# Kernel optimization log

Measured on AMD Instinct MI355X. Metric: run time of the kernel, lower is better.

The kernel has to match this reference:

```python
import jax, jax.numpy as jnp
import numpy as np

N = 50000          # nodes
E = 800000         # edges (before self-loops)
DIN = 1024         # input_dim_mel
HID = 128          # hidden_dim
HEADS = 2
NC = 4             # num_classes
NEG_SLOPE = 0.2    # PyG GATConv default


def setup_inputs() -> dict:
    key = jax.random.key(0)
    ks = jax.random.split(key, 12)
    s = 0.05
    return {
        "x": jax.random.normal(ks[0], (N, DIN), dtype=jnp.float32),
        "edge_index": jax.random.randint(ks[1], (2, E), 0, N, dtype=jnp.int64),
        # linear_pre (stored as [in, out])
        "W_pre": jax.random.normal(ks[2], (DIN, HID), dtype=jnp.float32) * s,
        "b_pre": jnp.zeros((HID,), dtype=jnp.float32),
        # gat1: GATConv(HID, HID, heads=2, concat=True)
        "W1": jax.random.normal(ks[3], (HID, HEADS * HID), dtype=jnp.float32) * s,
        "a_src1": jax.random.normal(ks[4], (HEADS, HID), dtype=jnp.float32) * s,
        "a_dst1": jax.random.normal(ks[5], (HEADS, HID), dtype=jnp.float32) * s,
        "b1": jnp.zeros((HEADS * HID,), dtype=jnp.float32),
        # gat2: GATConv(HID*HEADS, NC, heads=1, concat=True)
        "W2": jax.random.normal(ks[6], (HEADS * HID, NC), dtype=jnp.float32) * s,
        "a_src2": jax.random.normal(ks[7], (1, NC), dtype=jnp.float32) * s,
        "a_dst2": jax.random.normal(ks[8], (1, NC), dtype=jnp.float32) * s,
        "b2": jnp.zeros((NC,), dtype=jnp.float32),
    }


def _gat_conv(x, W, a_src, a_dst, bias, src, dst, heads, out_ch):
    """PyG GATConv (concat=True, self-loops already appended to src/dst)."""
    n = x.shape[0]
    h = (x @ W).reshape(n, heads, out_ch)            # [N,H,C]
    alpha_src = (h * a_src).sum(-1)                  # [N,H]
    alpha_dst = (h * a_dst).sum(-1)                  # [N,H]
    e = alpha_src[src] + alpha_dst[dst]              # [E,H] edge scores
    e = jax.nn.leaky_relu(e, NEG_SLOPE)
    # segment softmax over incoming edges of each dst node
    m = jax.ops.segment_max(e, dst, num_segments=n)  # [N,H]
    e = jnp.exp(e - m[dst])
    s = jax.ops.segment_sum(e, dst, num_segments=n)  # [N,H]
    alpha = e / (s[dst] + 1e-16)                     # [E,H]
    # gather src messages, weight by attention, scatter-add to dst
    out = jax.ops.segment_sum(h[src] * alpha[:, :, None], dst, num_segments=n)
    return out.reshape(n, heads * out_ch) + bias


def reference(x, edge_index, W_pre, b_pre, W1, a_src1, a_dst1, b1,
              W2, a_src2, a_dst2, b2):
    n = x.shape[0]
    # add self-loops (PyG GATConv default)
    loops = jnp.arange(n, dtype=edge_index.dtype)
    src = jnp.concatenate([edge_index[0], loops])
    dst = jnp.concatenate([edge_index[1], loops])

    h = jax.nn.relu(x @ W_pre + b_pre)                               # [N,HID]
    h = jax.nn.elu(_gat_conv(h, W1, a_src1, a_dst1, b1, src, dst, HEADS, HID))
    out = _gat_conv(h, W2, a_src2, a_dst2, b2, src, dst, 1, NC)      # [N,NC]
    return out
```

## Files before the change

### kernel.cpp

```cpp
#include <hip/hip_runtime.h>
#include <hip/hip_bf16.h>

#define NEG_SLOPE 0.2f

typedef _Float16 f16x8 __attribute__((ext_vector_type(8)));
typedef _Float16 f16x4 __attribute__((ext_vector_type(4)));
typedef float f32x4 __attribute__((ext_vector_type(4)));
typedef unsigned short ushort_t;

#define AS_GLOBAL(p) ((const __attribute__((address_space(1))) void*)(p))
#define AS_SHARED(p) ((__attribute__((address_space(3))) void*)(p))


__global__ void khist(const int* __restrict__ dst, int E, int* __restrict__ counts) {
    int i = blockIdx.x * blockDim.x + threadIdx.x;
    if (i < E) atomicAdd(&counts[dst[i]], 1);
}

__global__ __launch_bounds__(1024) void kscan_part(const int* __restrict__ counts,
                                                   int* __restrict__ row_ptr,
                                                   int* __restrict__ bsum, int n) {
    __shared__ int wsum[16];
    int t = threadIdx.x, lane = t & 63, wid = t >> 6;
    int i = blockIdx.x * 1024 + t;
    int v = (i < n) ? (counts[i] + 1) : 0;
    int x = v;
    #pragma unroll
    for (int off = 1; off < 64; off <<= 1) {
        int y = __shfl_up(x, off, 64);
        if (lane >= off) x += y;
    }
    if (lane == 63) wsum[wid] = x;
    __syncthreads();
    if (wid == 0) {
        int ws = (lane < 16) ? wsum[lane] : 0;
        #pragma unroll
        for (int off = 1; off < 16; off <<= 1) {
            int y = __shfl_up(ws, off, 64);
            if (lane >= off) ws += y;
        }
        if (lane < 16) wsum[lane] = ws;
    }
    __syncthreads();
    int wave_excl = (wid == 0) ? 0 : wsum[wid - 1];
    if (i < n) row_ptr[i] = wave_excl + (x - v);
    if (t == 0) bsum[blockIdx.x] = wsum[15];
}

__global__ void kscan_tops(const int* __restrict__ bsum, int* __restrict__ boff,
                           int* __restrict__ row_ptr, int G, int n) {
    int lane = threadIdx.x;
    int v = (lane < G) ? bsum[lane] : 0;
    int x = v;
    #pragma unroll
    for (int off = 1; off < 64; off <<= 1) {
        int y = __shfl_up(x, off, 64);
        if (lane >= off) x += y;
    }
    if (lane < G) boff[lane] = x - v;
    if (lane == 63) row_ptr[n] = x;
}

__global__ void kscan_add(int* __restrict__ row_ptr, const int* __restrict__ boff,
                          int* __restrict__ cursor, int n) {
    int i = blockIdx.x * blockDim.x + threadIdx.x;
    if (i < n) {
        int r = row_ptr[i] + boff[i >> 10];
        row_ptr[i] = r;
        cursor[i] = r;
    }
}

__global__ void kfill(const int* __restrict__ src, const int* __restrict__ dst,
                      int E, int n, int* __restrict__ cursor, int* __restrict__ edge_src) {
    int i = blockIdx.x * blockDim.x + threadIdx.x;
    if (i < E) {
        int p = atomicAdd(&cursor[dst[i]], 1);
        edge_src[p] = src[i];
    } else if (i < E + n) {
        int v = i - E;
        int p = atomicAdd(&cursor[v], 1);
        edge_src[p] = v;
    }
}

__global__ void kprep(const float* __restrict__ Wpre, const float* __restrict__ W1,
                      ushort_t* __restrict__ PreF, ushort_t* __restrict__ W1h) {
    int i = blockIdx.x * blockDim.x + threadIdx.x;
    if (i < 1024 * 128) {
        int k = i >> 7, n = i & 127;
        int d = ((k >> 3) * 128 + n) * 8 + (k & 7);
        PreF[d] = __builtin_bit_cast(ushort_t, (_Float16)Wpre[i]);
    } else if (i < 1024 * 128 + 128 * 256) {
        int j2 = i - 1024 * 128;
        int k = j2 >> 8, n = j2 & 255;
        int d = ((k >> 3) * 256 + n) * 8 + (k & 7);
        W1h[d] = __builtin_bit_cast(ushort_t, (_Float16)W1[j2]);
    }
}

__device__ inline f16x4 cvt4(float4 v) {
    f16x4 r;
    r[0] = (_Float16)v.x; r[1] = (_Float16)v.y;
    r[2] = (_Float16)v.z; r[3] = (_Float16)v.w;
    return r;
}

__global__ __launch_bounds__(256) void kgemm_mfma1(const float* __restrict__ A,
                                                   const ushort_t* __restrict__ Bf,
                                                   const float* __restrict__ bias,
                                                   ushort_t* __restrict__ C, int M) {
    __shared__ __align__(16) ushort_t Bs[8192];
    __shared__ __align__(16) ushort_t As[2048];
    int t = threadIdx.x;
    int wid = t >> 6, lane = t & 63, q = lane >> 4, l15 = lane & 15;
    int wr = wid & 1, wc = wid >> 1;
    int m0 = blockIdx.x * 32;

    int ar = t >> 3, ac = t & 7;
    int srow = m0 + ar;
    if (srow >= M) srow = M - 1;
    const float* sA = A + (size_t)srow * 1024;
    int sw = ar & 7;
    int wadr0 = ar * 64 + (((ac >> 1)) ^ sw) * 8 + (ac & 1) * 4;
    int wadr1 = ar * 64 + ((4 + (ac >> 1)) ^ sw) * 8 + (ac & 1) * 4;

    float4 av[2][2];
    av[0][0] = *(const float4*)(sA + ac * 4);
    av[0][1] = *(const float4*)(sA + 32 + ac * 4);

    f32x4 acc[4];
    #pragma unroll
    for (int c = 0; c < 4; ++c) acc[c] = (f32x4){0.f, 0.f, 0.f, 0.f};

    int arow_rd = (wr * 16 + l15) * 64;
    int asw = l15 & 7;

    #pragma unroll 2
    for (int kt = 0; kt < 16; ++kt) {
        int cur = kt & 1, nxt = cur ^ 1;
        __syncthreads();
        {
            const ushort_t* sF = Bf + kt * 8192;
            #pragma unroll
            for (int i = 0; i < 4; ++i) {
                int ge = (i * 256 + t) * 8;
                int le = (i * 256 + (t & 0xC0)) * 8;
                __builtin_amdgcn_global_load_lds(AS_GLOBAL(sF + ge), AS_SHARED(Bs + le), 16, 0, 0);
            }
        }
        if (kt < 15) {
            const float* a2 = sA + (kt + 1) * 64;
            av[nxt][0] = *(const float4*)(a2 + ac * 4);
            av[nxt][1] = *(const float4*)(a2 + 32 + ac * 4);
        }
        *(f16x4*)(As + wadr0) = cvt4(av[cur][0]);
        *(f16x4*)(As + wadr1) = cvt4(av[cur][1]);
        __syncthreads();
        #pragma unroll
        for (int ks = 0; ks < 2; ++ks) {
            int kc = ks * 4 + q;
            f16x8 af = *(const f16x8*)(As + arow_rd + ((kc ^ asw) * 8));
            #pragma unroll
            for (int c = 0; c < 4; ++c) {
                f16x8 b = *(const f16x8*)(Bs + (kc * 128 + wc * 64 + c * 16 + l15) * 8);
                acc[c] = __builtin_amdgcn_mfma_f32_16x16x32_f16(af, b, acc[c], 0, 0, 0);
            }
        }
    }
    #pragma unroll
    for (int c = 0; c < 4; ++c) {
        int n = wc * 64 + c * 16 + l15;
        float bv = bias[n];
        #pragma unroll
        for (int r = 0; r < 4; ++r) {
            int mm = m0 + wr * 16 + q * 4 + r;
            if (mm < M)
                C[(size_t)mm * 128 + n] =
                    __builtin_bit_cast(ushort_t, (_Float16)fmaxf(acc[c][r] + bv, 0.f));
        }
    }
}

__global__ __launch_bounds__(256) void kgemm_mfma2(const ushort_t* __restrict__ Ah,
                                                   const ushort_t* __restrict__ W1h,
                                                   const float* __restrict__ a_src,
                                                   const float* __restrict__ a_dst,
                                                   ushort_t* __restrict__ C,
                                                   float* __restrict__ as1,
                                                   float* __restrict__ ad1, int M) {
    __shared__ __align__(16) ushort_t Bs[16384];
    int t = threadIdx.x;
    int wid = t >> 6, lane = t & 63;
    int q = lane >> 4, l15 = lane & 15;
    int g = blockIdx.y;
    int m0 = blockIdx.x * 64 + wid * 16;
    int m = m0 + l15;
    const ushort_t* arow = Ah + (size_t)(m < M ? m : 0) * 128;

    {
        #pragma unroll
        for (int i = 0; i < 8; ++i) {
            int j = i * 4 + wid;
            int kc = j >> 1, hk = j & 1;
            int ge = ((kc * 256) + g * 128 + hk * 64 + lane) * 8;
            int le = j * 512;
            __builtin_amdgcn_global_load_lds(AS_GLOBAL(W1h + ge), AS_SHARED(Bs + le), 16, 0, 0);
        }
    }
    f16x8 af[4];
    #pragma unroll
    for (int ks = 0; ks < 4; ++ks)
        af[ks] = *(const f16x8*)(arow + ks * 32 + q * 8);
    __syncthreads();

    f32x4 acc[8];
    #pragma unroll
    for (int c = 0; c < 8; ++c) acc[c] = (f32x4){0.f, 0.f, 0.f, 0.f};

    #pragma unroll
    for (int ks = 0; ks < 4; ++ks) {
        int kc = ks * 4 + q;
        #pragma unroll
        for (int c = 0; c < 8; ++c) {
            f16x8 b = *(const f16x8*)(Bs + (kc * 128 + c * 16 + l15) * 8);
            acc[c] = __builtin_amdgcn_mfma_f32_16x16x32_f16(af[ks], b, acc[c], 0, 0, 0);
        }
    }
    #pragma unroll
    for (int c = 0; c < 8; ++c) {
        int n = g * 128 + c * 16 + l15;
        #pragma unroll
        for (int r = 0; r < 4; ++r) {
            int mm = m0 + q * 4 + r;
            if (mm < M)
                C[(size_t)mm * 256 + n] = __builtin_bit_cast(ushort_t, (_Float16)acc[c][r]);
        }
    }
    float asv[4] = {0.f, 0.f, 0.f, 0.f};
    float adv[4] = {0.f, 0.f, 0.f, 0.f};
    #pragma unroll
    for (int c = 0; c < 8; ++c) {
        float sa = a_src[g * 128 + c * 16 + l15];
        float da = a_dst[g * 128 + c * 16 + l15];
        #pragma unroll
        for (int r = 0; r < 4; ++r) {
            asv[r] += acc[c][r] * sa;
            adv[r] += acc[c][r] * da;
        }
    }
    #pragma unroll
    for (int off = 1; off <= 8; off <<= 1) {
        #pragma unroll
        for (int r = 0; r < 4; ++r) {
            asv[r] += __shfl_xor(asv[r], off, 64);
            adv[r] += __shfl_xor(adv[r], off, 64);
        }
    }
    if (l15 == 0) {
        #pragma unroll
        for (int r = 0; r < 4; ++r) {
            int node = m0 + q * 4 + r;
            if (node < M) {
                as1[node * 2 + g] = asv[r];
                ad1[node * 2 + g] = adv[r];
            }
        }
    }
}

__global__ __launch_bounds__(256) void kagg1(const ushort_t* __restrict__ h1h,
                                             const float* __restrict__ as1,
                                             const float* __restrict__ ad1,
                                             const float* __restrict__ b1,
                                             const float* __restrict__ W2,
                                             const float* __restrict__ a_src2,
                                             const float* __restrict__ a_dst2,
                                             const int* __restrict__ row_ptr,
                                             const int* __restrict__ edge_src,
                                             float* __restrict__ h2,
                                             float* __restrict__ as2,
                                             float* __restrict__ ad2, int n) {
    int wid = threadIdx.x >> 6, lane = threadIdx.x & 63;
    int node = blockIdx.x * 4 + wid;
    if (node >= n) return;
    int beg = row_ptr[node], end = row_ptr[node + 1];
    int h = lane >> 5;
    float adv0 = ad1[node * 2];
    float adv1 = ad1[node * 2 + 1];
    float acc0 = 0.f, acc1 = 0.f, acc2 = 0.f, acc3 = 0.f, ssum = 0.f;
    for (int base = beg; base < end; base += 32) {
        int cnt = min(32, end - base);
        float wv_mine = 0.f;
        int s_mine = 0;
        {
            int i = lane >> 1, hh = lane & 1;
            if (i < cnt) {
                s_mine = edge_src[base + i];
                float e = as1[s_mine * 2 + hh] + (hh ? adv1 : adv0);
                e = (e > 0.f) ? e : NEG_SLOPE * e;
                wv_mine = __expf(e);
            }
        }
        #pragma unroll 4
        for (int i2 = 0; i2 < cnt; ++i2) {
            int s = __shfl(s_mine, i2 * 2, 64);
            float wv = __shfl(wv_mine, i2 * 2 + h, 64);
            uint2 p = *(const uint2*)(h1h + (size_t)s * 256 + lane * 4);
            acc0 += wv * (float)__builtin_bit_cast(_Float16, (ushort_t)(p.x & 0xffffu));
            acc1 += wv * (float)__builtin_bit_cast(_Float16, (ushort_t)(p.x >> 16));
            acc2 += wv * (float)__builtin_bit_cast(_Float16, (ushort_t)(p.y & 0xffffu));
            acc3 += wv * (float)__builtin_bit_cast(_Float16, (ushort_t)(p.y >> 16));
            ssum += wv;
        }
    }
    float inv = 1.f / (ssum + 1e-16f);
    float o0 = acc0 * inv + b1[lane * 4 + 0];
    float o1 = acc1 * inv + b1[lane * 4 + 1];
    float o2 = acc2 * inv + b1[lane * 4 + 2];
    float o3 = acc3 * inv + b1[lane * 4 + 3];
    o0 = (o0 > 0.f) ? o0 : (__expf(o0) - 1.f);
    o1 = (o1 > 0.f) ? o1 : (__expf(o1) - 1.f);
    o2 = (o2 > 0.f) ? o2 : (__expf(o2) - 1.f);
    o3 = (o3 > 0.f) ? o3 : (__expf(o3) - 1.f);
    float4 w0 = *(const float4*)(W2 + (lane * 4 + 0) * 4);
    float4 w1 = *(const float4*)(W2 + (lane * 4 + 1) * 4);
    float4 w2 = *(const float4*)(W2 + (lane * 4 + 2) * 4);
    float4 w3 = *(const float4*)(W2 + (lane * 4 + 3) * 4);
    float p0 = o0 * w0.x + o1 * w1.x + o2 * w2.x + o3 * w3.x;
    float p1 = o0 * w0.y + o1 * w1.y + o2 * w2.y + o3 * w3.y;
    float p2 = o0 * w0.z + o1 * w1.z + o2 * w2.z + o3 * w3.z;
    float p3 = o0 * w0.w + o1 * w1.w + o2 * w2.w + o3 * w3.w;
    #pragma unroll
    for (int off = 1; off < 64; off <<= 1) {
        p0 += __shfl_xor(p0, off, 64);
        p1 += __shfl_xor(p1, off, 64);
        p2 += __shfl_xor(p2, off, 64);
        p3 += __shfl_xor(p3, off, 64);
    }
    if (lane == 0) {
        h2[node * 4 + 0] = p0;
        h2[node * 4 + 1] = p1;
        h2[node * 4 + 2] = p2;
        h2[node * 4 + 3] = p3;
        as2[node] = p0 * a_src2[0] + p1 * a_src2[1] + p2 * a_src2[2] + p3 * a_src2[3];
        ad2[node] = p0 * a_dst2[0] + p1 * a_dst2[1] + p2 * a_dst2[2] + p3 * a_dst2[3];
    }
}

__global__ __launch_bounds__(256) void kagg2(const float* __restrict__ h2,
                                             const float* __restrict__ as2,
                                             const float* __restrict__ ad2,
                                             const float* __restrict__ b2,
                                             const int* __restrict__ row_ptr,
                                             const int* __restrict__ edge_src,
                                             float* __restrict__ out, int n) {
    int wid = threadIdx.x >> 6, lane = threadIdx.x & 63;
    int node = blockIdx.x * 4 + wid;
    if (node >= n) return;
    int beg = row_ptr[node], end = row_ptr[node + 1];
    int j = lane & 3, ig = lane >> 2;
    float adv = ad2[node];
    float acc = 0.f, ssum = 0.f;
    for (int p = beg + ig; p < end; p += 16) {
        int s = edge_src[p];
        float e = as2[s] + adv;
        e = (e > 0.f) ? e : NEG_SLOPE * e;
        float wv = __expf(e);
        acc += wv * h2[s * 4 + j];
        ssum += wv;
    }
    #pragma unroll
    for (int off = 32; off >= 4; off >>= 1) {
        acc += __shfl_down(acc, off);
        ssum += __shfl_down(ssum, off);
    }
    if (lane < 4) out[node * 4 + j] = acc / (ssum + 1e-16f) + b2[j];
}

extern "C" void kernel_launch(void* const* d_in, const int* in_sizes, int n_in,
                              void* d_out, int out_size, void* d_ws, size_t ws_size,
                              hipStream_t stream) {
    const float* x      = (const float*)d_in[0];
    const int*   ei     = (const int*)d_in[1];
    const float* W_pre  = (const float*)d_in[2];
    const float* b_pre  = (const float*)d_in[3];
    const float* W1     = (const float*)d_in[4];
    const float* a_src1 = (const float*)d_in[5];
    const float* a_dst1 = (const float*)d_in[6];
    const float* b1     = (const float*)d_in[7];
    const float* W2     = (const float*)d_in[8];
    const float* a_src2 = (const float*)d_in[9];
    const float* a_dst2 = (const float*)d_in[10];
    const float* b2     = (const float*)d_in[11];
    float* out = (float*)d_out;

    const int DIN = 1024;
    const int E = in_sizes[1] / 2;
    const int N = in_sizes[0] / DIN;

    const int* esrc = ei;
    const int* edst = ei + E;

    char* ws = (char*)d_ws;
    size_t off = 0;
    ushort_t* h1h = (ushort_t*)(ws + off); off += (size_t)N * 256 * 2;
    ushort_t* h0h = (ushort_t*)(ws + off); off += (size_t)N * 128 * 2;
    float* as1 = (float*)(ws + off);  off += (size_t)N * 2 * 4;
    float* ad1 = (float*)(ws + off);  off += (size_t)N * 2 * 4;
    float* h2  = (float*)(ws + off);  off += (size_t)N * 4 * 4;
    float* as2 = (float*)(ws + off);  off += (size_t)N * 4;
    float* ad2 = (float*)(ws + off);  off += (size_t)N * 4;
    int* row_ptr = (int*)(ws + off);  off += ((size_t)N + 16) * 4;
    int* cursor  = (int*)(ws + off);  off += (size_t)N * 4;
    int* counts  = (int*)(ws + off);  off += (size_t)N * 4;
    int* bsum    = (int*)(ws + off);  off += 64 * 4;
    int* boff    = (int*)(ws + off);  off += 64 * 4;
    int* edge_src = (int*)(ws + off); off += (size_t)(E + N) * 4;
    ushort_t* PreF = (ushort_t*)(ws + off); off += 1024 * 128 * 2;
    ushort_t* W1h  = (ushort_t*)(ws + off); off += 128 * 256 * 2;

    int G = (N + 1023) / 1024;

    kprep<<<640, 256, 0, stream>>>(W_pre, W1, PreF, W1h);
    hipMemsetAsync(counts, 0, (size_t)N * 4, stream);
    khist<<<(E + 255) / 256, 256, 0, stream>>>(edst, E, counts);
    kscan_part<<<G, 1024, 0, stream>>>(counts, row_ptr, bsum, N);
    kscan_tops<<<1, 64, 0, stream>>>(bsum, boff, row_ptr, G, N);
    kscan_add<<<(N + 255) / 256, 256, 0, stream>>>(row_ptr, boff, cursor, N);
    kfill<<<(E + N + 255) / 256, 256, 0, stream>>>(esrc, edst, E, N, cursor, edge_src);

    int Mb32 = (N + 31) / 32;
    kgemm_mfma1<<<Mb32, 256, 0, stream>>>(x, PreF, b_pre, h0h, N);
    {
        int Mb = (N + 63) / 64;
        dim3 grid(Mb, 2);
        kgemm_mfma2<<<grid, 256, 0, stream>>>(h0h, W1h, a_src1, a_dst1, h1h, as1, ad1, N);
    }
    kagg1<<<(N + 3) / 4, 256, 0, stream>>>(h1h, as1, ad1, b1, W2, a_src2, a_dst2,
                                           row_ptr, edge_src, h2, as2, ad2, N);
    kagg2<<<(N + 3) / 4, 256, 0, stream>>>(h2, as2, ad2, b2, row_ptr, edge_src, out, N);
}
```

Baseline: 536.1 us.

## Merge CSR build kernels into GEMM launches to cut launch count

```diff
diff --git a/kernel.cpp b/kernel.cpp
--- a/kernel.cpp
+++ b/kernel.cpp
@@ -10,94 +10,6 @@
 
 #define AS_GLOBAL(p) ((const __attribute__((address_space(1))) void*)(p))
 #define AS_SHARED(p) ((__attribute__((address_space(3))) void*)(p))
-
-
-__global__ void khist(const int* __restrict__ dst, int E, int* __restrict__ counts) {
-    int i = blockIdx.x * blockDim.x + threadIdx.x;
-    if (i < E) atomicAdd(&counts[dst[i]], 1);
-}
-
-__global__ __launch_bounds__(1024) void kscan_part(const int* __restrict__ counts,
-                                                   int* __restrict__ row_ptr,
-                                                   int* __restrict__ bsum, int n) {
-    __shared__ int wsum[16];
-    int t = threadIdx.x, lane = t & 63, wid = t >> 6;
-    int i = blockIdx.x * 1024 + t;
-    int v = (i < n) ? (counts[i] + 1) : 0;
-    int x = v;
-    #pragma unroll
-    for (int off = 1; off < 64; off <<= 1) {
-        int y = __shfl_up(x, off, 64);
-        if (lane >= off) x += y;
-    }
-    if (lane == 63) wsum[wid] = x;
-    __syncthreads();
-    if (wid == 0) {
-        int ws = (lane < 16) ? wsum[lane] : 0;
-        #pragma unroll
-        for (int off = 1; off < 16; off <<= 1) {
-            int y = __shfl_up(ws, off, 64);
-            if (lane >= off) ws += y;
-        }
-        if (lane < 16) wsum[lane] = ws;
-    }
-    __syncthreads();
-    int wave_excl = (wid == 0) ? 0 : wsum[wid - 1];
-    if (i < n) row_ptr[i] = wave_excl + (x - v);
-    if (t == 0) bsum[blockIdx.x] = wsum[15];
-}
-
-__global__ void kscan_tops(const int* __restrict__ bsum, int* __restrict__ boff,
-                           int* __restrict__ row_ptr, int G, int n) {
-    int lane = threadIdx.x;
-    int v = (lane < G) ? bsum[lane] : 0;
-    int x = v;
-    #pragma unroll
-    for (int off = 1; off < 64; off <<= 1) {
-        int y = __shfl_up(x, off, 64);
-        if (lane >= off) x += y;
-    }
-    if (lane < G) boff[lane] = x - v;
-    if (lane == 63) row_ptr[n] = x;
-}
-
-__global__ void kscan_add(int* __restrict__ row_ptr, const int* __restrict__ boff,
-                          int* __restrict__ cursor, int n) {
-    int i = blockIdx.x * blockDim.x + threadIdx.x;
-    if (i < n) {
-        int r = row_ptr[i] + boff[i >> 10];
-        row_ptr[i] = r;
-        cursor[i] = r;
-    }
-}
-
-__global__ void kfill(const int* __restrict__ src, const int* __restrict__ dst,
-                      int E, int n, int* __restrict__ cursor, int* __restrict__ edge_src) {
-    int i = blockIdx.x * blockDim.x + threadIdx.x;
-    if (i < E) {
-        int p = atomicAdd(&cursor[dst[i]], 1);
-        edge_src[p] = src[i];
-    } else if (i < E + n) {
-        int v = i - E;
-        int p = atomicAdd(&cursor[v], 1);
-        edge_src[p] = v;
-    }
-}
-
-__global__ void kprep(const float* __restrict__ Wpre, const float* __restrict__ W1,
-                      ushort_t* __restrict__ PreF, ushort_t* __restrict__ W1h) {
-    int i = blockIdx.x * blockDim.x + threadIdx.x;
-    if (i < 1024 * 128) {
-        int k = i >> 7, n = i & 127;
-        int d = ((k >> 3) * 128 + n) * 8 + (k & 7);
-        PreF[d] = __builtin_bit_cast(ushort_t, (_Float16)Wpre[i]);
-    } else if (i < 1024 * 128 + 128 * 256) {
-        int j2 = i - 1024 * 128;
-        int k = j2 >> 8, n = j2 & 255;
-        int d = ((k >> 3) * 256 + n) * 8 + (k & 7);
-        W1h[d] = __builtin_bit_cast(ushort_t, (_Float16)W1[j2]);
-    }
-}
 
 __device__ inline f16x4 cvt4(float4 v) {
     f16x4 r;
@@ -106,16 +18,73 @@
     return r;
 }
 
-__global__ __launch_bounds__(256) void kgemm_mfma1(const float* __restrict__ A,
-                                                   const ushort_t* __restrict__ Bf,
-                                                   const float* __restrict__ bias,
-                                                   ushort_t* __restrict__ C, int M) {
+__global__ __launch_bounds__(256) void kl1(const int* __restrict__ edst, int E,
+                                           int* __restrict__ counts,
+                                           const float* __restrict__ Wpre,
+                                           const float* __restrict__ W1,
+                                           ushort_t* __restrict__ PreF,
+                                           ushort_t* __restrict__ W1h, int HB) {
+    int b = blockIdx.x, t = threadIdx.x;
+    if (b < HB) {
+        int i = b * 256 + t;
+        if (i < E) atomicAdd(&counts[edst[i]], 1);
+    } else {
+        int i = (b - HB) * 256 + t;
+        if (i < 1024 * 128) {
+            int k = i >> 7, n = i & 127;
+            int d = ((k >> 3) * 128 + n) * 8 + (k & 7);
+            PreF[d] = __builtin_bit_cast(ushort_t, (_Float16)Wpre[i]);
+        } else if (i < 1024 * 128 + 128 * 256) {
+            int j2 = i - 1024 * 128;
+            int k = j2 >> 8, n = j2 & 255;
+            int d = ((k >> 3) * 256 + n) * 8 + (k & 7);
+            W1h[d] = __builtin_bit_cast(ushort_t, (_Float16)W1[j2]);
+        }
+    }
+}
+
+__global__ __launch_bounds__(256) void kl2(const float* __restrict__ A,
+                                           const ushort_t* __restrict__ Bf,
+                                           const float* __restrict__ bias,
+                                           ushort_t* __restrict__ C, int M,
+                                           const int* __restrict__ counts,
+                                           int* __restrict__ row_ptr,
+                                           int* __restrict__ cursor) {
     __shared__ __align__(16) ushort_t Bs[8192];
     __shared__ __align__(16) ushort_t As[2048];
+    __shared__ int wsum2[4];
     int t = threadIdx.x;
+
+    if (blockIdx.x == 0) {
+        int CH = (M + 255) >> 8;
+        int lo = t * CH, hi = min(lo + CH, M);
+        int s = 0;
+        for (int i = lo; i < hi; ++i) s += counts[i] + 1;
+        int lane = t & 63, wid = t >> 6;
+        int x = s;
+        #pragma unroll
+        for (int off = 1; off < 64; off <<= 1) {
+            int y = __shfl_up(x, off, 64);
+            if (lane >= off) x += y;
+        }
+        if (lane == 63) wsum2[wid] = x;
+        __syncthreads();
+        int wof = 0;
+        #pragma unroll
+        for (int w = 0; w < 3; ++w) if (wid > w) wof += wsum2[w];
+        int run = wof + x - s;
+        for (int i = lo; i < hi; ++i) {
+            row_ptr[i] = run;
+            cursor[i] = run;
+            run += counts[i] + 1;
+        }
+        if (lo < M && hi == M) row_ptr[M] = run;
+        return;
+    }
+
     int wid = t >> 6, lane = t & 63, q = lane >> 4, l15 = lane & 15;
     int wr = wid & 1, wc = wid >> 1;
-    int m0 = blockIdx.x * 32;
+    int m0 = (blockIdx.x - 1) * 32;
 
     int ar = t >> 3, ac = t & 7;
     int srow = m0 + ar;
@@ -182,19 +151,38 @@
     }
 }
 
-__global__ __launch_bounds__(256) void kgemm_mfma2(const ushort_t* __restrict__ Ah,
-                                                   const ushort_t* __restrict__ W1h,
-                                                   const float* __restrict__ a_src,
-                                                   const float* __restrict__ a_dst,
-                                                   ushort_t* __restrict__ C,
-                                                   float* __restrict__ as1,
-                                                   float* __restrict__ ad1, int M) {
+__global__ __launch_bounds__(256) void kl3(const int* __restrict__ esrc,
+                                           const int* __restrict__ edst, int E, int n,
+                                           int* __restrict__ cursor,
+                                           int* __restrict__ edge_src, int FB,
+                                           const ushort_t* __restrict__ Ah,
+                                           const ushort_t* __restrict__ W1h,
+                                           const float* __restrict__ a_src,
+                                           const float* __restrict__ a_dst,
+                                           ushort_t* __restrict__ C,
+                                           float* __restrict__ as1,
+                                           float* __restrict__ ad1, int M) {
     __shared__ __align__(16) ushort_t Bs[16384];
     int t = threadIdx.x;
+    int b = blockIdx.x;
+    if (b < FB) {
+        int i = b * 256 + t;
+        if (i < E) {
+            int p = atomicAdd(&cursor[edst[i]], 1);
+            edge_src[p] = esrc[i];
+        } else if (i < E + n) {
+            int v = i - E;
+            int p = atomicAdd(&cursor[v], 1);
+            edge_src[p] = v;
+        }
+        return;
+    }
+    int u = b - FB;
+    int g = u & 1;
+    int mblk = u >> 1;
     int wid = t >> 6, lane = t & 63;
     int q = lane >> 4, l15 = lane & 15;
-    int g = blockIdx.y;
-    int m0 = blockIdx.x * 64 + wid * 16;
+    int m0 = mblk * 64 + wid * 16;
     int m = m0 + l15;
     const ushort_t* arow = Ah + (size_t)(m < M ? m : 0) * 128;
 
@@ -223,18 +211,18 @@
         int kc = ks * 4 + q;
         #pragma unroll
         for (int c = 0; c < 8; ++c) {
-            f16x8 b = *(const f16x8*)(Bs + (kc * 128 + c * 16 + l15) * 8);
-            acc[c] = __builtin_amdgcn_mfma_f32_16x16x32_f16(af[ks], b, acc[c], 0, 0, 0);
+            f16x8 bfr = *(const f16x8*)(Bs + (kc * 128 + c * 16 + l15) * 8);
+            acc[c] = __builtin_amdgcn_mfma_f32_16x16x32_f16(af[ks], bfr, acc[c], 0, 0, 0);
         }
     }
     #pragma unroll
     for (int c = 0; c < 8; ++c) {
-        int n = g * 128 + c * 16 + l15;
+        int nn = g * 128 + c * 16 + l15;
         #pragma unroll
         for (int r = 0; r < 4; ++r) {
             int mm = m0 + q * 4 + r;
             if (mm < M)
-                C[(size_t)mm * 256 + n] = __builtin_bit_cast(ushort_t, (_Float16)acc[c][r]);
+                C[(size_t)mm * 256 + nn] = __builtin_bit_cast(ushort_t, (_Float16)acc[c][r]);
         }
     }
     float asv[4] = {0.f, 0.f, 0.f, 0.f};
@@ -414,29 +402,23 @@
     int* row_ptr = (int*)(ws + off);  off += ((size_t)N + 16) * 4;
     int* cursor  = (int*)(ws + off);  off += (size_t)N * 4;
     int* counts  = (int*)(ws + off);  off += (size_t)N * 4;
-    int* bsum    = (int*)(ws + off);  off += 64 * 4;
-    int* boff    = (int*)(ws + off);  off += 64 * 4;
     int* edge_src = (int*)(ws + off); off += (size_t)(E + N) * 4;
     ushort_t* PreF = (ushort_t*)(ws + off); off += 1024 * 128 * 2;
     ushort_t* W1h  = (ushort_t*)(ws + off); off += 128 * 256 * 2;
 
-    int G = (N + 1023) / 1024;
-
-    kprep<<<640, 256, 0, stream>>>(W_pre, W1, PreF, W1h);
     hipMemsetAsync(counts, 0, (size_t)N * 4, stream);
-    khist<<<(E + 255) / 256, 256, 0, stream>>>(edst, E, counts);
-    kscan_part<<<G, 1024, 0, stream>>>(counts, row_ptr, bsum, N);
-    kscan_tops<<<1, 64, 0, stream>>>(bsum, boff, row_ptr, G, N);
-    kscan_add<<<(N + 255) / 256, 256, 0, stream>>>(row_ptr, boff, cursor, N);
-    kfill<<<(E + N + 255) / 256, 256, 0, stream>>>(esrc, edst, E, N, cursor, edge_src);
+
+    int HB = (E + 255) / 256;
+    kl1<<<HB + 640, 256, 0, stream>>>(edst, E, counts, W_pre, W1, PreF, W1h, HB);
 
     int Mb32 = (N + 31) / 32;
-    kgemm_mfma1<<<Mb32, 256, 0, stream>>>(x, PreF, b_pre, h0h, N);
-    {
-        int Mb = (N + 63) / 64;
-        dim3 grid(Mb, 2);
-        kgemm_mfma2<<<grid, 256, 0, stream>>>(h0h, W1h, a_src1, a_dst1, h1h, as1, ad1, N);
-    }
+    kl2<<<1 + Mb32, 256, 0, stream>>>(x, PreF, b_pre, h0h, N, counts, row_ptr, cursor);
+
+    int FB = (E + N + 255) / 256;
+    int Mb = (N + 63) / 64;
+    kl3<<<FB + 2 * Mb, 256, 0, stream>>>(esrc, edst, E, N, cursor, edge_src, FB,
+                                         h0h, W1h, a_src1, a_dst1, h1h, as1, ad1, N);
+
     kagg1<<<(N + 3) / 4, 256, 0, stream>>>(h1h, as1, ad1, b1, W2, a_src2, a_dst2,
                                            row_ptr, edge_src, h2, as2, ad2, N);
     kagg2<<<(N + 3) / 4, 256, 0, stream>>>(h2, as2, ad2, b2, row_ptr, edge_src, out, N);
```

After: 609.6 us. 13.7% more time.
